# Kernel tuning notes

Measured on AMD Instinct MI355X. Metric: run time of the kernel, lower is better.

Reference implementation:

```python
import jax, jax.numpy as jnp
import numpy as np

VOCAB = 150
EOS = 2
PAD = 0
EPS = 1e-8


def _ngram_penalty_sum(tokens, n):
    # tokens: [B, S] int. Returns sum over batch of (count-2)*0.1*n for each
    # ngram repeated >=3 times. Equivalent trick: hash each ngram to a unique
    # int (base-VOCAB encoding), sort per row; a position is a 3rd-or-later
    # occurrence iff sorted[i] == sorted[i-2]; the number of such positions
    # equals sum over unique ngrams of max(count-2, 0).
    B, S = tokens.shape
    if S < n * 3:
        return jnp.float32(0.0)
    L = S - n + 1
    h = sum(tokens[:, j:j + L].astype(jnp.int32) * (VOCAB ** j) for j in range(n))
    hs = jnp.sort(h, axis=1)
    rep = jnp.sum(hs[:, 2:] == hs[:, :-2], axis=1)  # [B]
    return jnp.sum(rep.astype(jnp.float32)) * (0.1 * n)


def setup_inputs() -> dict:
    key = jax.random.key(0)
    k1, k2, k3 = jax.random.split(key, 3)
    B, S, V, IN = 256, 512, VOCAB, 512
    predictions = jax.random.normal(k1, (B, S, V), dtype=jnp.float32)
    targets = jax.random.randint(k2, (B, S), 0, V)
    attention_weights = jax.random.uniform(k3, (B, S, IN), dtype=jnp.float32)
    return {"predictions": predictions, "targets": targets,
            "attention_weights": attention_weights}


def reference(predictions, targets, attention_weights):
    B, S, V = predictions.shape

    # --- main NLL loss (ignore_index=PAD, mean over non-pad) ---
    mask = (targets != PAD).astype(predictions.dtype)  # [B,S]
    gathered = jnp.take_along_axis(predictions, targets[..., None], axis=-1)[..., 0]
    main = -jnp.sum(gathered * mask) / jnp.maximum(jnp.sum(mask), 1.0)

    # --- pattern penalty on argmax tokens ---
    pred_tokens = jnp.argmax(predictions, axis=-1)  # [B,S]
    pattern = (_ngram_penalty_sum(pred_tokens, 2)
               + _ngram_penalty_sum(pred_tokens, 3)
               + _ngram_penalty_sum(pred_tokens, 4)) / B

    # --- EOS encouragement ---
    eos_mask = (targets == EOS).astype(predictions.dtype)  # [B,S]
    eos_probs = jax.nn.softmax(predictions, axis=-1)[:, :, EOS]  # [B,S]
    eos_loss = -jnp.mean(eos_mask * jnp.log(eos_probs + EPS))
    eos_loss = jnp.where(jnp.sum(eos_mask) > 0, eos_loss, 0.0)
    has_eos_t = jnp.any(targets == EOS, axis=1)
    has_eos_p = jnp.any(pred_tokens == EOS, axis=1)
    no_eos = jnp.mean((has_eos_t & ~has_eos_p).astype(predictions.dtype))
    eos_total = eos_loss + 0.5 * no_eos

    # --- attention diversity (negative mean entropy, scaled) ---
    ent = -jnp.sum(attention_weights * jnp.log(attention_weights + EPS), axis=-1)
    attention = -jnp.mean(ent) * 0.1

    total = main + 0.1 * pattern + 0.2 * eos_total + 0.05 * attention
    return jnp.stack([total, main, pattern, eos_total, attention])
```

## Files before the change

### kernel.cpp

```cpp
#include <hip/hip_runtime.h>
#include <math.h>

#define BB   256
#define SS   512
#define VV   150
#define INW  512
#define NPOS (BB * SS)
#define GRID_A 1024
#define GRID_B 2048
#define EPSF 1e-8f


__global__ __launch_bounds__(256) void kern_ab(
    const float* __restrict__ pred, const int* __restrict__ tgt,
    const float* __restrict__ attw, int* __restrict__ has_t,
    int* __restrict__ has_p, float4* __restrict__ pA,
    float* __restrict__ pB, unsigned char* __restrict__ toks)
{
    __shared__ float shp[16];
    const int tid  = threadIdx.x;
    const int lane = tid & 63;
    const int wid  = tid >> 6;

    if (blockIdx.x < GRID_A) {
        const int gw = blockIdx.x * 4 + wid;
        float s_g = 0.f, s_mc = 0.f, s_el = 0.f, s_ec = 0.f;
        #pragma unroll 1
        for (int it = 0; it < NPOS / (GRID_A * 4); ++it) {
            const int pos = gw + it * (GRID_A * 4);
            const float* row = pred + (size_t)pos * VV;
            const float v0 = row[lane];
            const float v1 = row[lane + 64];
            const bool  l3 = lane < (VV - 128);
            const float v2 = l3 ? row[lane + 128] : -INFINITY;

            float mv = v0; int mi = lane;
            if (v1 > mv) { mv = v1; mi = lane + 64; }
            if (v2 > mv) { mv = v2; mi = lane + 128; }
            #pragma unroll
            for (int off = 32; off > 0; off >>= 1) {
                float ov = __shfl_xor(mv, off);
                int   oi = __shfl_xor(mi, off);
                if (ov > mv || (ov == mv && oi < mi)) { mv = ov; mi = oi; }
            }

            float e = expf(v0 - mv) + expf(v1 - mv) + (l3 ? expf(v2 - mv) : 0.f);
            const int t = tgt[pos];
            float g = (lane == t) ? v0 : (lane + 64 == t) ? v1
                      : (l3 && lane + 128 == t) ? v2 : 0.f;
            #pragma unroll
            for (int off = 32; off > 0; off >>= 1) {
                e += __shfl_xor(e, off);
                g += __shfl_xor(g, off);
            }
            const float p2 = __shfl(v0, 2);

            if (lane == 0) {
                toks[pos] = (unsigned char)mi;
                const int b = pos >> 9;
                if (mi == 2) has_p[b] = 1;
                if (t == 2) {
                    has_t[b] = 1;
                    s_el += logf(expf(p2 - mv) / e + EPSF);
                    s_ec += 1.f;
                }
                if (t != 0) { s_g += g; s_mc += 1.f; }
            }
        }
        if (lane == 0) {
            shp[wid * 4 + 0] = s_g;  shp[wid * 4 + 1] = s_mc;
            shp[wid * 4 + 2] = s_el; shp[wid * 4 + 3] = s_ec;
        }
        __syncthreads();
        if (tid == 0) {
            float4 r;
            r.x = shp[0] + shp[4] + shp[8]  + shp[12];
            r.y = shp[1] + shp[5] + shp[9]  + shp[13];
            r.z = shp[2] + shp[6] + shp[10] + shp[14];
            r.w = shp[3] + shp[7] + shp[11] + shp[15];
            pA[blockIdx.x] = r;
        }
    } else {
        const int bb = blockIdx.x - GRID_A;
        const float4* a4 = (const float4*)attw;
        const size_t n4 = (size_t)BB * SS * INW / 4;
        const size_t stride = (size_t)GRID_B * 256;
        float s = 0.f;
        for (size_t i = (size_t)bb * 256 + tid; i < n4; i += stride) {
            float4 v = a4[i];
            s += v.x * logf(v.x + EPSF) + v.y * logf(v.y + EPSF)
               + v.z * logf(v.z + EPSF) + v.w * logf(v.w + EPSF);
        }
        #pragma unroll
        for (int off = 32; off > 0; off >>= 1) s += __shfl_xor(s, off);
        if (lane == 0) shp[wid] = s;
        __syncthreads();
        if (tid == 0) pB[bb] = shp[0] + shp[1] + shp[2] + shp[3];
    }
}

__global__ __launch_bounds__(256) void kern_c(
    const unsigned char* __restrict__ toks, int* __restrict__ pC)
{
    const int blk = blockIdx.x;
    const int b = blk & 255;
    const int n = 2 + (blk >> 8);
    const int L = SS - n + 1;

    __shared__ int tok[SS];
    __shared__ __align__(16) int h[SS];

    const unsigned char* rt = toks + b * SS;
    tok[threadIdx.x]       = rt[threadIdx.x];
    tok[threadIdx.x + 256] = rt[threadIdx.x + 256];
    __syncthreads();

    #pragma unroll
    for (int q = 0; q < 2; ++q) {
        const int i = threadIdx.x + q * 256;
        int hv;
        if (i < L) {
            hv = tok[i];
            int mul = VV;
            for (int j = 1; j < n; ++j) { hv += tok[i + j] * mul; mul *= VV; }
        } else {
            hv = 0x7F000000 + i;
        }
        h[i] = hv;
    }
    __syncthreads();

    const int i1 = threadIdx.x, i2 = threadIdx.x + 256;
    const int h1 = h[i1], h2 = h[i2];
    int c1 = 0, c2 = 0;
    #pragma unroll 4
    for (int j = 0; j < SS; j += 4) {
        const int4 hv = *(const int4*)&h[j];
        c1 += (hv.x == h1 && j     < i1) + (hv.y == h1 && j + 1 < i1)
            + (hv.z == h1 && j + 2 < i1) + (hv.w == h1 && j + 3 < i1);
        c2 += (hv.x == h2 && j     < i2) + (hv.y == h2 && j + 1 < i2)
            + (hv.z == h2 && j + 2 < i2) + (hv.w == h2 && j + 3 < i2);
    }
    int rep = (c1 >= 2) + (c2 >= 2);
    #pragma unroll
    for (int off = 32; off > 0; off >>= 1) rep += __shfl_xor(rep, off);
    __shared__ int w4[4];
    if ((threadIdx.x & 63) == 0) w4[threadIdx.x >> 6] = rep;
    __syncthreads();
    if (threadIdx.x == 0) pC[blk] = w4[0] + w4[1] + w4[2] + w4[3];
}

__global__ __launch_bounds__(256) void kern_f(
    const int* __restrict__ has_t, const int* __restrict__ has_p,
    const float4* __restrict__ pA, const float* __restrict__ pB,
    const int* __restrict__ pC, float* __restrict__ out)
{
    const int tid  = threadIdx.x;
    const int lane = tid & 63;
    const int wid  = tid >> 6;
    double v[9];
    #pragma unroll
    for (int k = 0; k < 9; ++k) v[k] = 0.0;

    for (int i = tid; i < GRID_A; i += 256) {
        const float4 p = pA[i];
        v[0] += p.x; v[1] += p.y; v[2] += p.z; v[3] += p.w;
    }
    for (int i = tid; i < GRID_B; i += 256) v[4] += pB[i];
    v[5] = pC[tid]; v[6] = pC[tid + 256]; v[7] = pC[tid + 512];
    v[8] = (has_t[tid] != 0 && has_p[tid] == 0) ? 1.0 : 0.0;

    #pragma unroll
    for (int off = 32; off > 0; off >>= 1)
        #pragma unroll
        for (int k = 0; k < 9; ++k) v[k] += __shfl_xor(v[k], off);

    __shared__ double sd[4][9];
    if (lane == 0)
        for (int k = 0; k < 9; ++k) sd[wid][k] = v[k];
    __syncthreads();

    if (tid == 0) {
        double r[9];
        for (int k = 0; k < 9; ++k) r[k] = sd[0][k] + sd[1][k] + sd[2][k] + sd[3][k];
        const double mainv    = -r[0] / fmax(r[1], 1.0);
        const double eos_loss = (r[3] > 0.0) ? (-r[2] / (double)NPOS) : 0.0;
        const double no_eos   = r[8] / (double)BB;
        const double eos_tot  = eos_loss + 0.5 * no_eos;
        const double att      = 0.1 * r[4] / (double)NPOS;
        const double pattern  = (0.2 * r[5] + 0.3 * r[6] + 0.4 * r[7]) / (double)BB;
        const double total    = mainv + 0.1 * pattern + 0.2 * eos_tot + 0.05 * att;
        out[0] = (float)total;   out[1] = (float)mainv; out[2] = (float)pattern;
        out[3] = (float)eos_tot; out[4] = (float)att;
    }
}

extern "C" void kernel_launch(void* const* d_in, const int* in_sizes, int n_in,
                              void* d_out, int out_size, void* d_ws, size_t ws_size,
                              hipStream_t stream)
{
    const float* pred = (const float*)d_in[0];
    const int*   tgt  = (const int*)d_in[1];
    const float* attw = (const float*)d_in[2];
    float* out = (float*)d_out;
    char*  ws  = (char*)d_ws;

    int*    has_t = (int*)ws;
    int*    has_p = (int*)(ws + 1024);
    float4* pA    = (float4*)(ws + 2048);
    float*  pB    = (float*)(ws + 18432);
    int*    pC    = (int*)(ws + 26624);
    unsigned char* toks = (unsigned char*)(ws + 29696);

    hipMemsetAsync(ws, 0, 2048, stream);
    kern_ab<<<GRID_A + GRID_B, 256, 0, stream>>>(pred, tgt, attw, has_t, has_p, pA, pB, toks);
    kern_c<<<768, 256, 0, stream>>>(toks, pC);
    kern_f<<<1, 256, 0, stream>>>(has_t, has_p, pA, pB, pC, out);
}
```

Measured before the change: 113.7 us.

## Streamline argmax/softmax path, move EOS flags to ngram kernel, drop memset

Splits the fused value/index argmax shuffle into a max reduction followed by a min-index reduction. The target logit is now fetched with a single shuffle, and the softmax denominator is computed only for rows whose target is EOS, using fast __expf/__logf intrinsics. The has-EOS flags move into the n-gram kernel, which removes the global flag writes and the memset launch. The attention-entropy loop gets a fixed trip count with unrolling. Fast-math intrinsics may shift results slightly.

Result: no change. 112.2 us (-1.3%).

```diff
diff --git a/kernel.cpp b/kernel.cpp
--- a/kernel.cpp
+++ b/kernel.cpp
@@ -13,8 +13,7 @@
 
 __global__ __launch_bounds__(256) void kern_ab(
     const float* __restrict__ pred, const int* __restrict__ tgt,
-    const float* __restrict__ attw, int* __restrict__ has_t,
-    int* __restrict__ has_p, float4* __restrict__ pA,
+    const float* __restrict__ attw, float4* __restrict__ pA,
     float* __restrict__ pB, unsigned char* __restrict__ toks)
 {
     __shared__ float shp[16];
@@ -25,7 +24,6 @@
     if (blockIdx.x < GRID_A) {
         const int gw = blockIdx.x * 4 + wid;
         float s_g = 0.f, s_mc = 0.f, s_el = 0.f, s_ec = 0.f;
-        #pragma unroll 1
         for (int it = 0; it < NPOS / (GRID_A * 4); ++it) {
             const int pos = gw + it * (GRID_A * 4);
             const float* row = pred + (size_t)pos * VV;
@@ -34,36 +32,34 @@
             const bool  l3 = lane < (VV - 128);
             const float v2 = l3 ? row[lane + 128] : -INFINITY;
 
-            float mv = v0; int mi = lane;
-            if (v1 > mv) { mv = v1; mi = lane + 64; }
-            if (v2 > mv) { mv = v2; mi = lane + 128; }
+            float m = fmaxf(fmaxf(v0, v1), v2);
             #pragma unroll
-            for (int off = 32; off > 0; off >>= 1) {
-                float ov = __shfl_xor(mv, off);
-                int   oi = __shfl_xor(mi, off);
-                if (ov > mv || (ov == mv && oi < mi)) { mv = ov; mi = oi; }
-            }
-
-            float e = expf(v0 - mv) + expf(v1 - mv) + (l3 ? expf(v2 - mv) : 0.f);
+            for (int off = 32; off > 0; off >>= 1)
+                m = fmaxf(m, __shfl_xor(m, off));
+            int li = (v0 == m) ? lane : (v1 == m) ? lane + 64
+                     : (l3 && v2 == m) ? lane + 128 : (1 << 20);
+            #pragma unroll
+            for (int off = 32; off > 0; off >>= 1)
+                li = min(li, __shfl_xor(li, off));
+
             const int t = tgt[pos];
-            float g = (lane == t) ? v0 : (lane + 64 == t) ? v1
-                      : (l3 && lane + 128 == t) ? v2 : 0.f;
-            #pragma unroll
-            for (int off = 32; off > 0; off >>= 1) {
-                e += __shfl_xor(e, off);
-                g += __shfl_xor(g, off);
-            }
-            const float p2 = __shfl(v0, 2);
-
-            if (lane == 0) {
-                toks[pos] = (unsigned char)mi;
-                const int b = pos >> 9;
-                if (mi == 2) has_p[b] = 1;
-                if (t == 2) {
-                    has_t[b] = 1;
-                    s_el += logf(expf(p2 - mv) / e + EPSF);
+            const float src = (t < 64) ? v0 : (t < 128) ? v1 : v2;
+            const float g = __shfl(src, t & 63);
+
+            if (t == 2) {
+                float ex = __expf(v0 - m) + __expf(v1 - m)
+                         + (l3 ? __expf(v2 - m) : 0.f);
+                #pragma unroll
+                for (int off = 32; off > 0; off >>= 1)
+                    ex += __shfl_xor(ex, off);
+                const float p2 = __shfl(v0, 2);
+                if (lane == 0) {
+                    s_el += __logf(__expf(p2 - m) / ex + EPSF);
                     s_ec += 1.f;
                 }
+            }
+            if (lane == 0) {
+                toks[pos] = (unsigned char)li;
                 if (t != 0) { s_g += g; s_mc += 1.f; }
             }
         }
@@ -83,13 +79,14 @@
     } else {
         const int bb = blockIdx.x - GRID_A;
         const float4* a4 = (const float4*)attw;
-        const size_t n4 = (size_t)BB * SS * INW / 4;
         const size_t stride = (size_t)GRID_B * 256;
+        const size_t i0 = (size_t)bb * 256 + tid;
         float s = 0.f;
-        for (size_t i = (size_t)bb * 256 + tid; i < n4; i += stride) {
-            float4 v = a4[i];
-            s += v.x * logf(v.x + EPSF) + v.y * logf(v.y + EPSF)
-               + v.z * logf(v.z + EPSF) + v.w * logf(v.w + EPSF);
+        #pragma unroll 4
+        for (int it = 0; it < 32; ++it) {
+            float4 v = a4[i0 + (size_t)it * stride];
+            s += v.x * __logf(v.x + EPSF) + v.y * __logf(v.y + EPSF)
+               + v.z * __logf(v.z + EPSF) + v.w * __logf(v.w + EPSF);
         }
         #pragma unroll
         for (int off = 32; off > 0; off >>= 1) s += __shfl_xor(s, off);
@@ -100,7 +97,8 @@
 }
 
 __global__ __launch_bounds__(256) void kern_c(
-    const unsigned char* __restrict__ toks, int* __restrict__ pC)
+    const unsigned char* __restrict__ toks, const int* __restrict__ tgt,
+    int* __restrict__ pC, int* __restrict__ hasx)
 {
     const int blk = blockIdx.x;
     const int b = blk & 255;
@@ -109,11 +107,21 @@
 
     __shared__ int tok[SS];
     __shared__ __align__(16) int h[SS];
-
+    __shared__ int sflags;
+
+    if (threadIdx.x == 0) sflags = 0;
     const unsigned char* rt = toks + b * SS;
     tok[threadIdx.x]       = rt[threadIdx.x];
     tok[threadIdx.x + 256] = rt[threadIdx.x + 256];
     __syncthreads();
+
+    if (blk < 256) {
+        const int* trow = tgt + b * SS;
+        int f = 0;
+        if (trow[threadIdx.x] == 2 || trow[threadIdx.x + 256] == 2) f |= 1;
+        if (tok[threadIdx.x] == 2 || tok[threadIdx.x + 256] == 2)   f |= 2;
+        if (f) atomicOr(&sflags, f);
+    }
 
     #pragma unroll
     for (int q = 0; q < 2; ++q) {
@@ -147,13 +155,16 @@
     __shared__ int w4[4];
     if ((threadIdx.x & 63) == 0) w4[threadIdx.x >> 6] = rep;
     __syncthreads();
-    if (threadIdx.x == 0) pC[blk] = w4[0] + w4[1] + w4[2] + w4[3];
+    if (threadIdx.x == 0) {
+        pC[blk] = w4[0] + w4[1] + w4[2] + w4[3];
+        if (blk < 256) hasx[b] = ((sflags & 1) && !(sflags & 2)) ? 1 : 0;
+    }
 }
 
 __global__ __launch_bounds__(256) void kern_f(
-    const int* __restrict__ has_t, const int* __restrict__ has_p,
-    const float4* __restrict__ pA, const float* __restrict__ pB,
-    const int* __restrict__ pC, float* __restrict__ out)
+    const int* __restrict__ hasx, const float4* __restrict__ pA,
+    const float* __restrict__ pB, const int* __restrict__ pC,
+    float* __restrict__ out)
 {
     const int tid  = threadIdx.x;
     const int lane = tid & 63;
@@ -168,7 +179,7 @@
     }
     for (int i = tid; i < GRID_B; i += 256) v[4] += pB[i];
     v[5] = pC[tid]; v[6] = pC[tid + 256]; v[7] = pC[tid + 512];
-    v[8] = (has_t[tid] != 0 && has_p[tid] == 0) ? 1.0 : 0.0;
+    v[8] = (double)hasx[tid];
 
     #pragma unroll
     for (int off = 32; off > 0; off >>= 1)
@@ -205,15 +216,13 @@
     float* out = (float*)d_out;
     char*  ws  = (char*)d_ws;
 
-    int*    has_t = (int*)ws;
-    int*    has_p = (int*)(ws + 1024);
-    float4* pA    = (float4*)(ws + 2048);
-    float*  pB    = (float*)(ws + 18432);
-    int*    pC    = (int*)(ws + 26624);
-    unsigned char* toks = (unsigned char*)(ws + 29696);
-
-    hipMemsetAsync(ws, 0, 2048, stream);
-    kern_ab<<<GRID_A + GRID_B, 256, 0, stream>>>(pred, tgt, attw, has_t, has_p, pA, pB, toks);
-    kern_c<<<768, 256, 0, stream>>>(toks, pC);
-    kern_f<<<1, 256, 0, stream>>>(has_t, has_p, pA, pB, pC, out);
-}
+    float4* pA   = (float4*)ws;
+    float*  pB   = (float*)(ws + 16384);
+    int*    pC   = (int*)(ws + 24576);
+    int*    hasx = (int*)(ws + 27648);
+    unsigned char* toks = (unsigned char*)(ws + 28672);
+
+    kern_ab<<<GRID_A + GRID_B, 256, 0, stream>>>(pred, tgt, attw, pA, pB, toks);
+    kern_c<<<768, 256, 0, stream>>>(toks, tgt, pC, hasx);
+    kern_f<<<1, 256, 0, stream>>>(hasx, pA, pB, pC, out);
+}
```
